# Kernel optimization log

Hardware: AMD Instinct MI355X
Metric: run time of the kernel (lower is better)

Reference implementation:

```python
import jax, jax.numpy as jnp
import numpy as np

D_MODEL, N_HEADS, D_FF = 512, 8, 2048
B, L = 2, 2048


def layer_norm(x, g, b, eps=1e-5):
    mu = jnp.mean(x, axis=-1, keepdims=True)
    var = jnp.mean(jnp.square(x - mu), axis=-1, keepdims=True)
    return (x - mu) * jax.lax.rsqrt(var + eps) * g + b


def setup_inputs() -> dict:
    key = jax.random.key(0)
    ks = jax.random.split(key, 16)
    s = 1.0 / np.sqrt(D_MODEL)
    sf = 1.0 / np.sqrt(D_FF)
    return {
        "x": jax.random.normal(ks[0], (B, L, D_MODEL), jnp.float32),
        "Wq": jax.random.normal(ks[1], (D_MODEL, D_MODEL), jnp.float32) * s,
        "bq": jnp.zeros((D_MODEL,), jnp.float32),
        "Wk": jax.random.normal(ks[2], (D_MODEL, D_MODEL), jnp.float32) * s,
        "bk": jnp.zeros((D_MODEL,), jnp.float32),
        "Wv": jax.random.normal(ks[3], (D_MODEL, D_MODEL), jnp.float32) * s,
        "bv": jnp.zeros((D_MODEL,), jnp.float32),
        "Wo": jax.random.normal(ks[4], (D_MODEL, D_MODEL), jnp.float32) * s,
        "bo": jnp.zeros((D_MODEL,), jnp.float32),
        "W1": jax.random.normal(ks[5], (D_FF, D_MODEL), jnp.float32) * s,   # conv1 k=1 -> linear
        "b1": jnp.zeros((D_FF,), jnp.float32),
        "W2": jax.random.normal(ks[6], (D_MODEL, D_FF), jnp.float32) * sf,  # conv2 k=1 -> linear
        "b2": jnp.zeros((D_MODEL,), jnp.float32),
        "g1": jnp.ones((D_MODEL,), jnp.float32),
        "be1": jnp.zeros((D_MODEL,), jnp.float32),
        "g2": jnp.ones((D_MODEL,), jnp.float32),
        "be2": jnp.zeros((D_MODEL,), jnp.float32),
    }


def reference(x, Wq, bq, Wk, bk, Wv, bv, Wo, bo, W1, b1, W2, b2, g1, be1, g2, be2):
    Bx, Lx, D = x.shape
    H = N_HEADS
    dk = D // H
    # projections -> [B, L, H, dk]
    q = (x @ Wq.T + bq).reshape(Bx, Lx, H, dk)
    k = (x @ Wk.T + bk).reshape(Bx, Lx, H, dk)
    v = (x @ Wv.T + bv).reshape(Bx, Lx, H, dk)
    scale = 1.0 / jnp.sqrt(jnp.asarray(dk, x.dtype))
    scores = jnp.einsum('blhd,bshd->bhls', q, k)  # full LxL score tensor (as in source)
    A = jax.nn.softmax(scale * scores, axis=-1)
    out = jnp.einsum('bhls,bshd->blhd', A, v).reshape(Bx, Lx, D)
    attn_out = out @ Wo.T + bo
    # residual + norm1 (dropout is identity in eval)
    x1 = layer_norm(x + attn_out, g1, be1)
    # FFN: conv1d with kernel_size=1 == pointwise linear
    y = jax.nn.relu(x1 @ W1.T + b1)
    y = y @ W2.T + b2
    return layer_norm(x1 + y, g2, be2)
```

## Files before the change

### kernel.cpp

```cpp
#include <hip/hip_runtime.h>
#include <hip/hip_bf16.h>
#include <cstddef>

#define SEQ 2048
#define DM  512
#define NH  8
#define DKH 64
#define DFF 2048
#define NB  2
#define MR  (NB*SEQ)

typedef __attribute__((ext_vector_type(8)))  short short8;
typedef __attribute__((ext_vector_type(4)))  float f32x4;
typedef __attribute__((ext_vector_type(16))) float f32x16;

#define AS1(p) ((const __attribute__((address_space(1))) void*)(p))
#define AS3(p) ((__attribute__((address_space(3))) void*)(p))

#define QSCALE 0.180336880f

__device__ inline unsigned cvtpk(float lo, float hi) {
  unsigned r;
  asm("v_cvt_pk_bf16_f32 %0, %1, %2" : "=v"(r) : "v"(lo), "v"(hi));
  return r;
}

__device__ inline void cvt8(const float* __restrict__ s, __hip_bfloat16* __restrict__ d) {
  float4 a = *reinterpret_cast<const float4*>(s);
  float4 b = *reinterpret_cast<const float4*>(s + 4);
  union { __hip_bfloat16 h[8]; short8 v; } u;
  u.h[0] = __float2bfloat16(a.x); u.h[1] = __float2bfloat16(a.y);
  u.h[2] = __float2bfloat16(a.z); u.h[3] = __float2bfloat16(a.w);
  u.h[4] = __float2bfloat16(b.x); u.h[5] = __float2bfloat16(b.y);
  u.h[6] = __float2bfloat16(b.z); u.h[7] = __float2bfloat16(b.w);
  *reinterpret_cast<short8*>(d) = u.v;
}

__global__ __launch_bounds__(256) void cvt_all(
    const float* __restrict__ x,
    const float* __restrict__ Wq, const float* __restrict__ Wk,
    const float* __restrict__ Wv, const float* __restrict__ Wo,
    const float* __restrict__ W1, const float* __restrict__ W2,
    const float* __restrict__ bq, const float* __restrict__ bk,
    const float* __restrict__ bv,
    __hip_bfloat16* __restrict__ xb,  __hip_bfloat16* __restrict__ wqkv,
    __hip_bfloat16* __restrict__ wob, __hip_bfloat16* __restrict__ w1b,
    __hip_bfloat16* __restrict__ w2b, float* __restrict__ bqkv)
{
  const int u = blockIdx.x * 256 + threadIdx.x;
  if (u < 262144) {
    cvt8(x + (size_t)u * 8, xb + (size_t)u * 8);
  } else if (u < 360448) {
    const int d = (u - 262144) * 8;
    const int n = d >> 9, k = d & 511;
    const float* src = (n < 512) ? (Wq + (size_t)n * 512 + k)
                     : (n < 1024) ? (Wk + (size_t)(n - 512) * 512 + k)
                                  : (Wv + (size_t)(n - 1024) * 512 + k);
    cvt8(src, wqkv + d);
  } else if (u < 393216) {
    const int d = (u - 360448) * 8; cvt8(Wo + d, wob + d);
  } else if (u < 524288) {
    const int d = (u - 393216) * 8; cvt8(W1 + d, w1b + d);
  } else if (u < 655360) {
    const int d = (u - 524288) * 8; cvt8(W2 + d, w2b + d);
  } else if (u < 655552) {
    const int d = (u - 655360) * 8;
    const float* src = (d < 512) ? (bq + d) : (d < 1024) ? (bk + d - 512) : (bv + d - 1024);
    *reinterpret_cast<float4*>(bqkv + d)     = *reinterpret_cast<const float4*>(src);
    *reinterpret_cast<float4*>(bqkv + d + 4) = *reinterpret_cast<const float4*>(src + 4);
  }
}

template<int OUT_BF16, int RELU, int WVT, int SPLITK>
__global__ __launch_bounds__(256) void gemm_bt(
    const __hip_bfloat16* __restrict__ A, const __hip_bfloat16* __restrict__ Bt,
    const float* __restrict__ bias, void* __restrict__ Cout, void* __restrict__ Cout1,
    __hip_bfloat16* __restrict__ qkbO, __hip_bfloat16* __restrict__ vtO,
    int M, int N, int K)
{
  __shared__ __align__(16) char lds[32768];
  char* Asm = lds;
  char* Bsm = lds + 16384;
  const int t = threadIdx.x, lane = t & 63, w = t >> 6;
  const int m0 = blockIdx.y * 128, n0 = blockIdx.x * 128;
  const int wm = w >> 1, wn = w & 1;
  const int z = (SPLITK == 2) ? blockIdx.z : 0;
  const int Keff = (SPLITK == 2) ? (K >> 1) : K;
  const int koff = z * Keff;
  const int g = lane >> 4;

  const int r0   = t >> 3;
  const int kofs = ((lane & 7) ^ (r0 & 7)) * 8;
  const __hip_bfloat16* ap = A  + (size_t)(m0 + r0) * K + koff + kofs;
  const __hip_bfloat16* bp = Bt + (size_t)(n0 + r0) * K + koff + kofs;
  const int ldsoff = t * 16;

  const int fA = (wm * 64 + (lane & 15)) * 128;
  const int fB = (wn * 64 + (lane & 15)) * 128;
  const int sw = lane & 7;

  f32x4 acc[4][4] = {};

  const int nkt = Keff >> 6;
  for (int kt = 0; kt < nkt; ++kt) {
    const size_t ko = (size_t)kt * 64;
#pragma unroll
    for (int ii = 0; ii < 4; ++ii) {
      __builtin_amdgcn_global_load_lds(AS1(ap + (size_t)ii * 32 * K + ko), AS3(Asm + ii * 4096 + ldsoff), 16, 0, 0);
      __builtin_amdgcn_global_load_lds(AS1(bp + (size_t)ii * 32 * K + ko), AS3(Bsm + ii * 4096 + ldsoff), 16, 0, 0);
    }
    __syncthreads();
#pragma unroll
    for (int kk = 0; kk < 2; ++kk) {
      const int cx = ((kk * 4 + g) ^ sw) * 16;
      short8 af[4], bf[4];
#pragma unroll
      for (int i = 0; i < 4; ++i) af[i] = *reinterpret_cast<const short8*>(Asm + fA + i * 2048 + cx);
#pragma unroll
      for (int j = 0; j < 4; ++j) bf[j] = *reinterpret_cast<const short8*>(Bsm + fB + j * 2048 + cx);
      __builtin_amdgcn_s_setprio(1);
#pragma unroll
      for (int i = 0; i < 4; ++i)
#pragma unroll
        for (int j = 0; j < 4; ++j)
          acc[i][j] = __builtin_amdgcn_mfma_f32_16x16x32_bf16(af[i], bf[j], acc[i][j], 0, 0, 0);
      __builtin_amdgcn_s_setprio(0);
    }
    __syncthreads();
  }

  float bcol[4];
#pragma unroll
  for (int j = 0; j < 4; ++j)
    bcol[j] = (SPLITK == 2 && z) ? 0.f : bias[n0 + wn * 64 + j * 16 + (lane & 15)];

  if (WVT && n0 >= 1024) {
#pragma unroll
    for (int i = 0; i < 4; ++i) {
      const int r = m0 + wm * 64 + i * 16 + (g << 2);
      const int bb = r >> 11, s = r & 2047;
#pragma unroll
      for (int j = 0; j < 4; ++j) {
        const int hd = n0 + wn * 64 + j * 16 + (lane & 15) - 1024;
        union { __hip_bfloat16 h[4]; uint2 uu; } pk;
#pragma unroll
        for (int jj = 0; jj < 4; ++jj) pk.h[jj] = __float2bfloat16(acc[i][j][jj] + bcol[j]);
        *reinterpret_cast<uint2*>(vtO + ((size_t)(bb * 8 + (hd >> 6)) * 64 + (hd & 63)) * SEQ + s) = pk.uu;
      }
    }
    return;
  }

  const float qsc = (WVT && n0 < 512) ? QSCALE : 1.0f;
#pragma unroll
  for (int i = 0; i < 4; ++i) {
    const int row = m0 + wm * 64 + i * 16 + (g << 2);
#pragma unroll
    for (int j = 0; j < 4; ++j) {
      const int col = n0 + wn * 64 + j * 16 + (lane & 15);
#pragma unroll
      for (int jj = 0; jj < 4; ++jj) {
        float v = acc[i][j][jj] + bcol[j];
        if (RELU) v = fmaxf(v, 0.f);
        if (WVT)
          qkbO[(size_t)(row + jj) * 1024 + col] = __float2bfloat16(v * qsc);
        else if (OUT_BF16)
          ((__hip_bfloat16*)Cout)[(size_t)(row + jj) * N + col] = __float2bfloat16(v);
        else {
          float* dst = (float*)((SPLITK == 2 && z) ? Cout1 : Cout);
          dst[(size_t)(row + jj) * N + col] = v;
        }
      }
    }
  }
}

__global__ __launch_bounds__(256) void attn_mfma(
    const __hip_bfloat16* __restrict__ qkb, const __hip_bfloat16* __restrict__ vtb,
    __hip_bfloat16* __restrict__ po, float* __restrict__ pm, float* __restrict__ pl)
{
  __shared__ __align__(16) char lds[24576];
  char* ks = lds;
  char* vT = lds + 16384;

  const int t = threadIdx.x, lane = t & 63, w = t >> 6;
  const int qt = blockIdx.x, bh = blockIdx.y, z = blockIdx.z;
  const int b = bh >> 3, h = bh & 7;
  const int ST0 = z * (SEQ / 4);
  const int NT = SEQ / 4 / 64;
  const int l31 = lane & 31, hi = lane >> 5;
  const int swz = (lane & 7) << 4;
  const int hi16 = hi * 16;

  const __hip_bfloat16* Qg = qkb + (size_t)b * SEQ * 1024 + h * DKH;
  const int qrow = qt * 128 + w * 32 + l31;
  short8 qf[4];
#pragma unroll
  for (int kc = 0; kc < 4; ++kc)
    qf[kc] = *reinterpret_cast<const short8*>(Qg + (size_t)qrow * 1024 + kc * 16 + hi * 8);

  const int srow = t >> 3;
  const int sofs = ((lane & 7) ^ (srow & 7)) * 8;
  const __hip_bfloat16* kbase = qkb + (size_t)(b * SEQ + ST0 + srow) * 1024 + 512 + h * DKH + sofs;
  const __hip_bfloat16* vbase = vtb + ((size_t)bh * 64 + srow) * SEQ + ST0 + sofs;
  const int ldso = t * 16;

  f32x16 o0 = {}, o1 = {};
  float m_ = -1e30f, l_ = 0.f;

  auto STAGE_K = [&](int buf, int st) {
    const size_t ko = (size_t)st * 64 * 1024;
    char* kd = ks + buf * 8192 + ldso;
    __builtin_amdgcn_global_load_lds(AS1(kbase + ko),                     AS3(kd),        16, 0, 0);
    __builtin_amdgcn_global_load_lds(AS1(kbase + ko + (size_t)32 * 1024), AS3(kd + 4096), 16, 0, 0);
  };
  auto STAGE_V = [&](int st) {
    const size_t vo = (size_t)st * 64;
    char* vd = vT + ldso;
    __builtin_amdgcn_global_load_lds(AS1(vbase + vo),                    AS3(vd),        16, 0, 0);
    __builtin_amdgcn_global_load_lds(AS1(vbase + vo + (size_t)32 * SEQ), AS3(vd + 4096), 16, 0, 0);
  };

  STAGE_K(0, 0);
  __syncthreads();
  int cur = 0;

  for (int st = 0; st < NT; ++st) {
    STAGE_V(st);
    STAGE_K(cur ^ 1, st + 1 < NT ? st + 1 : st);
    const char* kb_ = ks + cur * 8192;

    f32x16 acc0 = {}, acc1 = {};
    __builtin_amdgcn_s_setprio(1);
#pragma unroll
    for (int kc = 0; kc < 4; ++kc) {
      const int kbyte = (kc * 32 + hi16) ^ swz;
      const short8 ka0 = *reinterpret_cast<const short8*>(kb_ + l31 * 128 + kbyte);
      const short8 ka1 = *reinterpret_cast<const short8*>(kb_ + (32 + l31) * 128 + kbyte);
      acc0 = __builtin_amdgcn_mfma_f32_32x32x16_bf16(ka0, qf[kc], acc0, 0, 0, 0);
      acc1 = __builtin_amdgcn_mfma_f32_32x32x16_bf16(ka1, qf[kc], acc1, 0, 0, 0);
    }
    __builtin_amdgcn_s_setprio(0);

    float tm[16];
#pragma unroll
    for (int r = 0; r < 16; ++r) tm[r] = fmaxf(acc0[r], acc1[r]);
#pragma unroll
    for (int sft = 8; sft >= 1; sft >>= 1)
#pragma unroll
      for (int r = 0; r < sft; ++r) tm[r] = fmaxf(tm[r], tm[r + sft]);
    float pmax = fmaxf(tm[0], __shfl_xor(tm[0], 32));

    const bool skip = __all(pmax <= m_ + 8.0f);
    float al = 1.0f;
    if (!skip) {
      const float mn = fmaxf(m_, pmax);
      al = exp2f(m_ - mn);
      m_ = mn;
    }

    short8 pf[4];
    float ps = 0.f;
#pragma unroll
    for (int sc = 0; sc < 4; ++sc) {
      const f32x16& A = (sc < 2) ? acc0 : acc1;
      const int rb = (sc & 1) * 8;
      float e0 = exp2f(A[rb+0] - m_), e1 = exp2f(A[rb+1] - m_);
      float e2 = exp2f(A[rb+2] - m_), e3 = exp2f(A[rb+3] - m_);
      float e4 = exp2f(A[rb+4] - m_), e5 = exp2f(A[rb+5] - m_);
      float e6 = exp2f(A[rb+6] - m_), e7 = exp2f(A[rb+7] - m_);
      ps += ((e0 + e1) + (e2 + e3)) + ((e4 + e5) + (e6 + e7));
      unsigned w0 = cvtpk(e0, e1), w1 = cvtpk(e2, e3);
      unsigned w2 = cvtpk(e4, e5), w3 = cvtpk(e6, e7);
      asm("v_permlane32_swap_b32 %0, %1" : "+v"(w0), "+v"(w2));
      asm("v_permlane32_swap_b32 %0, %1" : "+v"(w1), "+v"(w3));
      union { unsigned u[4]; short8 s8; } pu;
      pu.u[0] = w0; pu.u[1] = w1; pu.u[2] = w2; pu.u[3] = w3;
      pf[sc] = pu.s8;
    }
    ps += __shfl_xor(ps, 32);
    l_ = l_ * al + ps;
    if (!skip) {
#pragma unroll
      for (int r = 0; r < 16; ++r) { o0[r] *= al; o1[r] *= al; }
    }

    asm volatile("s_waitcnt vmcnt(2)" ::: "memory");
    __builtin_amdgcn_s_barrier();
    __builtin_amdgcn_sched_barrier(0);

    __builtin_amdgcn_s_setprio(1);
#pragma unroll
    for (int sc = 0; sc < 4; ++sc) {
      const int sbyte = (sc * 32 + hi16) ^ swz;
      const short8 va0 = *reinterpret_cast<const short8*>(vT + l31 * 128 + sbyte);
      const short8 va1 = *reinterpret_cast<const short8*>(vT + (32 + l31) * 128 + sbyte);
      o0 = __builtin_amdgcn_mfma_f32_32x32x16_bf16(va0, pf[sc], o0, 0, 0, 0);
      o1 = __builtin_amdgcn_mfma_f32_32x32x16_bf16(va1, pf[sc], o1, 0, 0, 0);
    }
    __builtin_amdgcn_s_setprio(0);
    __syncthreads();
    cur ^= 1;
  }

  {
    __hip_bfloat16* pz = po + (size_t)z * MR * DM;
    const size_t orow = (size_t)b * SEQ + qt * 128 + w * 32 + l31;
    __hip_bfloat16* dst = pz + orow * DM + h * DKH;
#pragma unroll
    for (int r = 0; r < 4; ++r) {
      uint2 u0, u1;
      u0.x = cvtpk(o0[4*r+0], o0[4*r+1]); u0.y = cvtpk(o0[4*r+2], o0[4*r+3]);
      u1.x = cvtpk(o1[4*r+0], o1[4*r+1]); u1.y = cvtpk(o1[4*r+2], o1[4*r+3]);
      *reinterpret_cast<uint2*>(dst + r * 8 + hi * 4)      = u0;
      *reinterpret_cast<uint2*>(dst + 32 + r * 8 + hi * 4) = u1;
    }
  }
  if (lane < 32) {
    const size_t idx = ((size_t)z * 16 + bh) * SEQ + qt * 128 + w * 32 + lane;
    pm[idx] = m_;
    pl[idx] = l_;
  }
}

__global__ __launch_bounds__(256) void attn_combine(
    const __hip_bfloat16* __restrict__ po, const float* __restrict__ pm,
    const float* __restrict__ pl, __hip_bfloat16* __restrict__ attnb)
{
  const int row  = blockIdx.x * 4 + (threadIdx.x >> 6);
  const int lane = threadIdx.x & 63;
  const int d0 = lane * 8, h = lane >> 3;
  const int b = row >> 11, qq = row & 2047;
  const size_t idx = ((size_t)b * 8 + h) * SEQ + qq;
  const size_t zs = (size_t)16 * SEQ;
  const float m0 = pm[idx], m1 = pm[idx + zs], m2 = pm[idx + 2*zs], m3 = pm[idx + 3*zs];
  const float l0 = pl[idx], l1 = pl[idx + zs], l2 = pl[idx + 2*zs], l3 = pl[idx + 3*zs];
  const float M = fmaxf(fmaxf(m0, m1), fmaxf(m2, m3));
  const float a0 = exp2f(m0 - M), a1 = exp2f(m1 - M);
  const float a2 = exp2f(m2 - M), a3 = exp2f(m3 - M);
  const float inv = 1.0f / (l0*a0 + l1*a1 + l2*a2 + l3*a3);
  float az[4] = {a0, a1, a2, a3};
  float acc[8] = {};
  const size_t ro = (size_t)row * DM + d0;
#pragma unroll
  for (int zz = 0; zz < 4; ++zz) {
    short8 v = *reinterpret_cast<const short8*>(po + (size_t)zz * MR * DM + ro);
#pragma unroll
    for (int j = 0; j < 8; ++j) {
      const unsigned uu = ((unsigned)(unsigned short)v[j]) << 16;
      acc[j] += az[zz] * __builtin_bit_cast(float, uu);
    }
  }
  union { __hip_bfloat16 hh[8]; short8 s8; } u;
#pragma unroll
  for (int j = 0; j < 8; ++j) u.hh[j] = __float2bfloat16(acc[j] * inv);
  *reinterpret_cast<short8*>(attnb + ro) = u.s8;
}

template<int WB>
__global__ __launch_bounds__(256) void ln_res(
    const float* __restrict__ X, const float* __restrict__ Y0,
    const float* __restrict__ Y1,
    const float* __restrict__ g, const float* __restrict__ be,
    float* __restrict__ out, __hip_bfloat16* __restrict__ outb)
{
  const int row  = blockIdx.x * 4 + (threadIdx.x >> 6);
  const int lane = threadIdx.x & 63;
  const int c0   = lane * 8;
  const float* xr = X  + (size_t)row * DM;
  const float* y0 = Y0 + (size_t)row * DM;
  const float* y1 = Y1 + (size_t)row * DM;

  float v[8];
  float4 a0 = *reinterpret_cast<const float4*>(xr + c0);
  float4 a1 = *reinterpret_cast<const float4*>(xr + c0 + 4);
  float4 b0 = *reinterpret_cast<const float4*>(y0 + c0);
  float4 b1 = *reinterpret_cast<const float4*>(y0 + c0 + 4);
  float4 c0v= *reinterpret_cast<const float4*>(y1 + c0);
  float4 c1v= *reinterpret_cast<const float4*>(y1 + c0 + 4);
  v[0]=a0.x+b0.x+c0v.x; v[1]=a0.y+b0.y+c0v.y; v[2]=a0.z+b0.z+c0v.z; v[3]=a0.w+b0.w+c0v.w;
  v[4]=a1.x+b1.x+c1v.x; v[5]=a1.y+b1.y+c1v.y; v[6]=a1.z+b1.z+c1v.z; v[7]=a1.w+b1.w+c1v.w;

  float s = 0.f;
#pragma unroll
  for (int i = 0; i < 8; ++i) s += v[i];
#pragma unroll
  for (int off = 32; off >= 1; off >>= 1) s += __shfl_xor(s, off);
  const float mu = s * (1.0f/512.0f);

  float ss = 0.f;
#pragma unroll
  for (int i = 0; i < 8; ++i) { const float d = v[i] - mu; ss += d*d; }
#pragma unroll
  for (int off = 32; off >= 1; off >>= 1) ss += __shfl_xor(ss, off);
  const float rs = rsqrtf(ss * (1.0f/512.0f) + 1e-5f);

  float4 g0 = *reinterpret_cast<const float4*>(g  + c0);
  float4 g1 = *reinterpret_cast<const float4*>(g  + c0 + 4);
  float4 e0 = *reinterpret_cast<const float4*>(be + c0);
  float4 e1 = *reinterpret_cast<const float4*>(be + c0 + 4);
  float r[8];
  r[0]=(v[0]-mu)*rs*g0.x+e0.x; r[1]=(v[1]-mu)*rs*g0.y+e0.y;
  r[2]=(v[2]-mu)*rs*g0.z+e0.z; r[3]=(v[3]-mu)*rs*g0.w+e0.w;
  r[4]=(v[4]-mu)*rs*g1.x+e1.x; r[5]=(v[5]-mu)*rs*g1.y+e1.y;
  r[6]=(v[6]-mu)*rs*g1.z+e1.z; r[7]=(v[7]-mu)*rs*g1.w+e1.w;
  float4 o0, o1;
  o0.x=r[0]; o0.y=r[1]; o0.z=r[2]; o0.w=r[3];
  o1.x=r[4]; o1.y=r[5]; o1.z=r[6]; o1.w=r[7];
  *reinterpret_cast<float4*>(out + (size_t)row * DM + c0)     = o0;
  *reinterpret_cast<float4*>(out + (size_t)row * DM + c0 + 4) = o1;
  if (WB) {
    union { __hip_bfloat16 h[8]; short8 vv; } u;
#pragma unroll
    for (int i = 0; i < 8; ++i) u.h[i] = __float2bfloat16(r[i]);
    *reinterpret_cast<short8*>(outb + (size_t)row * DM + c0) = u.vv;
  }
}

extern "C" void kernel_launch(void* const* d_in, const int* in_sizes, int n_in,
                              void* d_out, int out_size, void* d_ws, size_t ws_size,
                              hipStream_t stream)
{
  const float* x   = (const float*)d_in[0];
  const float* Wq  = (const float*)d_in[1];
  const float* bq  = (const float*)d_in[2];
  const float* Wk  = (const float*)d_in[3];
  const float* bk  = (const float*)d_in[4];
  const float* Wv  = (const float*)d_in[5];
  const float* bv  = (const float*)d_in[6];
  const float* Wo  = (const float*)d_in[7];
  const float* bo  = (const float*)d_in[8];
  const float* W1  = (const float*)d_in[9];
  const float* b1  = (const float*)d_in[10];
  const float* W2  = (const float*)d_in[11];
  const float* b2  = (const float*)d_in[12];
  const float* g1  = (const float*)d_in[13];
  const float* be1 = (const float*)d_in[14];
  const float* g2  = (const float*)d_in[15];
  const float* be2 = (const float*)d_in[16];
  float* out = (float*)d_out;

  char* p = (char*)d_ws;
  __hip_bfloat16* xb    = (__hip_bfloat16*)p;  p += 4194304;
  __hip_bfloat16* wqkv  = (__hip_bfloat16*)p;  p += 1572864;
  __hip_bfloat16* wob   = (__hip_bfloat16*)p;  p += 524288;
  __hip_bfloat16* w1b   = (__hip_bfloat16*)p;  p += 2097152;
  __hip_bfloat16* w2b   = (__hip_bfloat16*)p;  p += 2097152;
  float*          bqkv  = (float*)p;           p += 8192;
  __hip_bfloat16* qkb   = (__hip_bfloat16*)p;  p += 8388608;
  __hip_bfloat16* vtb   = (__hip_bfloat16*)p;  p += 4194304;
  __hip_bfloat16* pob   = (__hip_bfloat16*)p;  p += 16777216;
  float*          pm    = (float*)p;           p += 524288;
  float*          pl    = (float*)p;           p += 524288;
  float*          oproj = (float*)p;           p += 8388608;
  __hip_bfloat16* x1b   = (__hip_bfloat16*)p;  p += 4194304;

  float*          x1    = (float*)qkb;
  __hip_bfloat16* attnb = (__hip_bfloat16*)vtb;
  float*          opa   = (float*)pob;
  __hip_bfloat16* f1b   = pob;
  float*          y2a   = (float*)d_ws;
  float*          y2b   = oproj;

  const dim3 blk(256);

  cvt_all<<<dim3(2561), blk, 0, stream>>>(x, Wq, Wk, Wv, Wo, W1, W2, bq, bk, bv,
                                          xb, wqkv, wob, w1b, w2b, bqkv);
  gemm_bt<1,0,1,0><<<dim3(12, 32), blk, 0, stream>>>(xb, wqkv, bqkv, nullptr, nullptr, qkb, vtb, MR, 1536, DM);
  attn_mfma   <<<dim3(SEQ/128, NB*NH, 4), blk, 0, stream>>>(qkb, vtb, pob, pm, pl);
  attn_combine<<<dim3(MR/4), blk, 0, stream>>>(pob, pm, pl, attnb);
  gemm_bt<0,0,0,2><<<dim3(4, 32, 2), blk, 0, stream>>>(attnb, wob, bo, opa, oproj, nullptr, nullptr, MR, DM, DM);
  ln_res<1><<<dim3(MR/4), blk, 0, stream>>>(x, opa, oproj, g1, be1, x1, x1b);
  gemm_bt<1,1,0,0><<<dim3(16, 32), blk, 0, stream>>>(x1b, w1b, b1, f1b, nullptr, nullptr, nullptr, MR, DFF, DM);
  gemm_bt<0,0,0,2><<<dim3(4, 32, 2), blk, 0, stream>>>(f1b, w2b, b2, y2a, y2b, nullptr, nullptr, MR, DM, DFF);
  ln_res<0><<<dim3(MR/4), blk, 0, stream>>>(x1, y2a, y2b, g2, be2, out, nullptr);
}
```

Measured before the change: 134.5 us.

## Double-buffer GEMM K-tiles and attention V tiles, split attention into half-tiles

The GEMM loop now uses two 16KB LDS buffers with 32-wide K tiles and a 4-chunk swizzle. The next tile is prefetched while the current one is consumed, removing one barrier per iteration. The attention kernel double-buffers V alongside K, drops the mid-loop vmcnt wait and barrier, and handles each 64-key tile as two 32-key halves so softmax and PV run per half with fewer live registers. The cost is more LDS in attention (32KB), twice as many K iterations in the GEMM, and extra online-softmax rescale steps.

```diff
diff --git a/kernel.cpp b/kernel.cpp
--- a/kernel.cpp
+++ b/kernel.cpp
@@ -79,8 +79,6 @@
     int M, int N, int K)
 {
   __shared__ __align__(16) char lds[32768];
-  char* Asm = lds;
-  char* Bsm = lds + 16384;
   const int t = threadIdx.x, lane = t & 63, w = t >> 6;
   const int m0 = blockIdx.y * 128, n0 = blockIdx.x * 128;
   const int wm = w >> 1, wn = w & 1;
@@ -89,44 +87,52 @@
   const int koff = z * Keff;
   const int g = lane >> 4;
 
-  const int r0   = t >> 3;
-  const int kofs = ((lane & 7) ^ (r0 & 7)) * 8;
-  const __hip_bfloat16* ap = A  + (size_t)(m0 + r0) * K + koff + kofs;
-  const __hip_bfloat16* bp = Bt + (size_t)(n0 + r0) * K + koff + kofs;
+  const int r0   = t >> 2;
+  const int kofs = ((lane & 3) ^ (r0 & 3)) * 8;
+  const __hip_bfloat16* a0 = A  + (size_t)(m0 + r0)      * K + koff + kofs;
+  const __hip_bfloat16* a1 = A  + (size_t)(m0 + r0 + 64) * K + koff + kofs;
+  const __hip_bfloat16* b0 = Bt + (size_t)(n0 + r0)      * K + koff + kofs;
+  const __hip_bfloat16* b1 = Bt + (size_t)(n0 + r0 + 64) * K + koff + kofs;
   const int ldsoff = t * 16;
 
-  const int fA = (wm * 64 + (lane & 15)) * 128;
-  const int fB = (wn * 64 + (lane & 15)) * 128;
-  const int sw = lane & 7;
+  const int ca = (lane >> 4) ^ (lane & 3);
+  const int fA = (wm * 64 + (lane & 15)) * 64 + ca * 16;
+  const int fB = (wn * 64 + (lane & 15)) * 64 + ca * 16;
 
   f32x4 acc[4][4] = {};
-
-  const int nkt = Keff >> 6;
+  const int nkt = Keff >> 5;
+
+  auto STAGE = [&](int buf, int kt) {
+    const size_t ko = (size_t)kt * 32;
+    char* bb = lds + buf * 16384;
+    __builtin_amdgcn_global_load_lds(AS1(a0 + ko), AS3(bb + ldsoff),         16, 0, 0);
+    __builtin_amdgcn_global_load_lds(AS1(a1 + ko), AS3(bb + 4096  + ldsoff), 16, 0, 0);
+    __builtin_amdgcn_global_load_lds(AS1(b0 + ko), AS3(bb + 8192  + ldsoff), 16, 0, 0);
+    __builtin_amdgcn_global_load_lds(AS1(b1 + ko), AS3(bb + 12288 + ldsoff), 16, 0, 0);
+  };
+
+  STAGE(0, 0);
+  __syncthreads();
+  int cur = 0;
+
   for (int kt = 0; kt < nkt; ++kt) {
-    const size_t ko = (size_t)kt * 64;
-#pragma unroll
-    for (int ii = 0; ii < 4; ++ii) {
-      __builtin_amdgcn_global_load_lds(AS1(ap + (size_t)ii * 32 * K + ko), AS3(Asm + ii * 4096 + ldsoff), 16, 0, 0);
-      __builtin_amdgcn_global_load_lds(AS1(bp + (size_t)ii * 32 * K + ko), AS3(Bsm + ii * 4096 + ldsoff), 16, 0, 0);
-    }
+    STAGE(cur ^ 1, kt + 1 < nkt ? kt + 1 : kt);
+    const char* Ab = lds + cur * 16384;
+    const char* Bb = Ab + 8192;
+    short8 af[4], bf[4];
+#pragma unroll
+    for (int i = 0; i < 4; ++i) af[i] = *reinterpret_cast<const short8*>(Ab + fA + i * 1024);
+#pragma unroll
+    for (int j = 0; j < 4; ++j) bf[j] = *reinterpret_cast<const short8*>(Bb + fB + j * 1024);
+    __builtin_amdgcn_s_setprio(1);
+#pragma unroll
+    for (int i = 0; i < 4; ++i)
+#pragma unroll
+      for (int j = 0; j < 4; ++j)
+        acc[i][j] = __builtin_amdgcn_mfma_f32_16x16x32_bf16(af[i], bf[j], acc[i][j], 0, 0, 0);
+    __builtin_amdgcn_s_setprio(0);
     __syncthreads();
-#pragma unroll
-    for (int kk = 0; kk < 2; ++kk) {
-      const int cx = ((kk * 4 + g) ^ sw) * 16;
-      short8 af[4], bf[4];
-#pragma unroll
-      for (int i = 0; i < 4; ++i) af[i] = *reinterpret_cast<const short8*>(Asm + fA + i * 2048 + cx);
-#pragma unroll
-      for (int j = 0; j < 4; ++j) bf[j] = *reinterpret_cast<const short8*>(Bsm + fB + j * 2048 + cx);
-      __builtin_amdgcn_s_setprio(1);
-#pragma unroll
-      for (int i = 0; i < 4; ++i)
-#pragma unroll
-        for (int j = 0; j < 4; ++j)
-          acc[i][j] = __builtin_amdgcn_mfma_f32_16x16x32_bf16(af[i], bf[j], acc[i][j], 0, 0, 0);
-      __builtin_amdgcn_s_setprio(0);
-    }
-    __syncthreads();
+    cur ^= 1;
   }
 
   float bcol[4];
@@ -179,7 +185,7 @@
     const __hip_bfloat16* __restrict__ qkb, const __hip_bfloat16* __restrict__ vtb,
     __hip_bfloat16* __restrict__ po, float* __restrict__ pm, float* __restrict__ pl)
 {
-  __shared__ __align__(16) char lds[24576];
+  __shared__ __align__(16) char lds[32768];
   char* ks = lds;
   char* vT = lds + 16384;
 
@@ -214,91 +220,93 @@
     __builtin_amdgcn_global_load_lds(AS1(kbase + ko),                     AS3(kd),        16, 0, 0);
     __builtin_amdgcn_global_load_lds(AS1(kbase + ko + (size_t)32 * 1024), AS3(kd + 4096), 16, 0, 0);
   };
-  auto STAGE_V = [&](int st) {
+  auto STAGE_V = [&](int buf, int st) {
     const size_t vo = (size_t)st * 64;
-    char* vd = vT + ldso;
+    char* vd = vT + buf * 8192 + ldso;
     __builtin_amdgcn_global_load_lds(AS1(vbase + vo),                    AS3(vd),        16, 0, 0);
     __builtin_amdgcn_global_load_lds(AS1(vbase + vo + (size_t)32 * SEQ), AS3(vd + 4096), 16, 0, 0);
   };
 
   STAGE_K(0, 0);
+  STAGE_V(0, 0);
   __syncthreads();
   int cur = 0;
 
   for (int st = 0; st < NT; ++st) {
-    STAGE_V(st);
-    STAGE_K(cur ^ 1, st + 1 < NT ? st + 1 : st);
+    const int nxt = st + 1 < NT ? st + 1 : st;
+    STAGE_V(cur ^ 1, nxt);
+    STAGE_K(cur ^ 1, nxt);
     const char* kb_ = ks + cur * 8192;
-
-    f32x16 acc0 = {}, acc1 = {};
-    __builtin_amdgcn_s_setprio(1);
-#pragma unroll
-    for (int kc = 0; kc < 4; ++kc) {
-      const int kbyte = (kc * 32 + hi16) ^ swz;
-      const short8 ka0 = *reinterpret_cast<const short8*>(kb_ + l31 * 128 + kbyte);
-      const short8 ka1 = *reinterpret_cast<const short8*>(kb_ + (32 + l31) * 128 + kbyte);
-      acc0 = __builtin_amdgcn_mfma_f32_32x32x16_bf16(ka0, qf[kc], acc0, 0, 0, 0);
-      acc1 = __builtin_amdgcn_mfma_f32_32x32x16_bf16(ka1, qf[kc], acc1, 0, 0, 0);
+    const char* vb_ = vT + cur * 8192;
+
+#pragma unroll
+    for (int half = 0; half < 2; ++half) {
+      const int rbase = (half * 32 + l31) * 128;
+
+      f32x16 acc = {};
+      __builtin_amdgcn_s_setprio(1);
+#pragma unroll
+      for (int kc = 0; kc < 4; ++kc) {
+        const int kbyte = (kc * 32 + hi16) ^ swz;
+        const short8 ka = *reinterpret_cast<const short8*>(kb_ + rbase + kbyte);
+        acc = __builtin_amdgcn_mfma_f32_32x32x16_bf16(ka, qf[kc], acc, 0, 0, 0);
+      }
+      __builtin_amdgcn_s_setprio(0);
+
+      float tm[8];
+#pragma unroll
+      for (int r = 0; r < 8; ++r) tm[r] = fmaxf(acc[r], acc[r + 8]);
+#pragma unroll
+      for (int sft = 4; sft >= 1; sft >>= 1)
+#pragma unroll
+        for (int r = 0; r < sft; ++r) tm[r] = fmaxf(tm[r], tm[r + sft]);
+      float pmax = fmaxf(tm[0], __shfl_xor(tm[0], 32));
+
+      const bool skip = __all(pmax <= m_ + 8.0f);
+      float al = 1.0f;
+      if (!skip) {
+        const float mn = fmaxf(m_, pmax);
+        al = exp2f(m_ - mn);
+        m_ = mn;
+      }
+
+      short8 pf[2];
+      float ps = 0.f;
+#pragma unroll
+      for (int sc = 0; sc < 2; ++sc) {
+        const int rb = sc * 8;
+        float e0 = exp2f(acc[rb+0] - m_), e1 = exp2f(acc[rb+1] - m_);
+        float e2 = exp2f(acc[rb+2] - m_), e3 = exp2f(acc[rb+3] - m_);
+        float e4 = exp2f(acc[rb+4] - m_), e5 = exp2f(acc[rb+5] - m_);
+        float e6 = exp2f(acc[rb+6] - m_), e7 = exp2f(acc[rb+7] - m_);
+        ps += ((e0 + e1) + (e2 + e3)) + ((e4 + e5) + (e6 + e7));
+        unsigned w0 = cvtpk(e0, e1), w1 = cvtpk(e2, e3);
+        unsigned w2 = cvtpk(e4, e5), w3 = cvtpk(e6, e7);
+        asm("v_permlane32_swap_b32 %0, %1" : "+v"(w0), "+v"(w2));
+        asm("v_permlane32_swap_b32 %0, %1" : "+v"(w1), "+v"(w3));
+        union { unsigned u[4]; short8 s8; } pu;
+        pu.u[0] = w0; pu.u[1] = w1; pu.u[2] = w2; pu.u[3] = w3;
+        pf[sc] = pu.s8;
+      }
+      ps += __shfl_xor(ps, 32);
+      l_ = l_ * al + ps;
+      if (!skip) {
+#pragma unroll
+        for (int r = 0; r < 16; ++r) { o0[r] *= al; o1[r] *= al; }
+      }
+
+      __builtin_amdgcn_s_setprio(1);
+#pragma unroll
+      for (int kc = 0; kc < 2; ++kc) {
+        const int sbyte = (half * 64 + kc * 32 + hi16) ^ swz;
+        const short8 va0 = *reinterpret_cast<const short8*>(vb_ + l31 * 128 + sbyte);
+        const short8 va1 = *reinterpret_cast<const short8*>(vb_ + (32 + l31) * 128 + sbyte);
+        o0 = __builtin_amdgcn_mfma_f32_32x32x16_bf16(va0, pf[kc], o0, 0, 0, 0);
+        o1 = __builtin_amdgcn_mfma_f32_32x32x16_bf16(va1, pf[kc], o1, 0, 0, 0);
+      }
+      __builtin_amdgcn_s_setprio(0);
     }
-    __builtin_amdgcn_s_setprio(0);
-
-    float tm[16];
-#pragma unroll
-    for (int r = 0; r < 16; ++r) tm[r] = fmaxf(acc0[r], acc1[r]);
-#pragma unroll
-    for (int sft = 8; sft >= 1; sft >>= 1)
-#pragma unroll
-      for (int r = 0; r < sft; ++r) tm[r] = fmaxf(tm[r], tm[r + sft]);
-    float pmax = fmaxf(tm[0], __shfl_xor(tm[0], 32));
-
-    const bool skip = __all(pmax <= m_ + 8.0f);
-    float al = 1.0f;
-    if (!skip) {
-      const float mn = fmaxf(m_, pmax);
-      al = exp2f(m_ - mn);
-      m_ = mn;
-    }
-
-    short8 pf[4];
-    float ps = 0.f;
-#pragma unroll
-    for (int sc = 0; sc < 4; ++sc) {
-      const f32x16& A = (sc < 2) ? acc0 : acc1;
-      const int rb = (sc & 1) * 8;
-      float e0 = exp2f(A[rb+0] - m_), e1 = exp2f(A[rb+1] - m_);
-      float e2 = exp2f(A[rb+2] - m_), e3 = exp2f(A[rb+3] - m_);
-      float e4 = exp2f(A[rb+4] - m_), e5 = exp2f(A[rb+5] - m_);
-      float e6 = exp2f(A[rb+6] - m_), e7 = exp2f(A[rb+7] - m_);
-      ps += ((e0 + e1) + (e2 + e3)) + ((e4 + e5) + (e6 + e7));
-      unsigned w0 = cvtpk(e0, e1), w1 = cvtpk(e2, e3);
-      unsigned w2 = cvtpk(e4, e5), w3 = cvtpk(e6, e7);
-      asm("v_permlane32_swap_b32 %0, %1" : "+v"(w0), "+v"(w2));
-      asm("v_permlane32_swap_b32 %0, %1" : "+v"(w1), "+v"(w3));
-      union { unsigned u[4]; short8 s8; } pu;
-      pu.u[0] = w0; pu.u[1] = w1; pu.u[2] = w2; pu.u[3] = w3;
-      pf[sc] = pu.s8;
-    }
-    ps += __shfl_xor(ps, 32);
-    l_ = l_ * al + ps;
-    if (!skip) {
-#pragma unroll
-      for (int r = 0; r < 16; ++r) { o0[r] *= al; o1[r] *= al; }
-    }
-
-    asm volatile("s_waitcnt vmcnt(2)" ::: "memory");
-    __builtin_amdgcn_s_barrier();
-    __builtin_amdgcn_sched_barrier(0);
-
-    __builtin_amdgcn_s_setprio(1);
-#pragma unroll
-    for (int sc = 0; sc < 4; ++sc) {
-      const int sbyte = (sc * 32 + hi16) ^ swz;
-      const short8 va0 = *reinterpret_cast<const short8*>(vT + l31 * 128 + sbyte);
-      const short8 va1 = *reinterpret_cast<const short8*>(vT + (32 + l31) * 128 + sbyte);
-      o0 = __builtin_amdgcn_mfma_f32_32x32x16_bf16(va0, pf[sc], o0, 0, 0, 0);
-      o1 = __builtin_amdgcn_mfma_f32_32x32x16_bf16(va1, pf[sc], o1, 0, 0, 0);
-    }
-    __builtin_amdgcn_s_setprio(0);
+
     __syncthreads();
     cur ^= 1;
   }
```

Result: no change. 133.3 us (-0.9%).
